# Performance work log

Measured on AMD Instinct MI355X. Metric: run time of the kernel, lower is better.

The kernel has to match this reference:

```python
import jax, jax.numpy as jnp
import numpy as np

N = 50000        # nodes
E = 1_000_000    # edges
F_IN = 128       # input features
H1, D1 = 8, 16   # layer-1 heads / per-head dim
D2 = 2           # layer-2 out dim (heads=1, concat=False)
NEG_SLOPE = 0.2  # PyG GATConv default leaky-relu slope


def setup_inputs() -> dict:
    key = jax.random.key(0)
    ks = jax.random.split(key, 10)
    x = jax.random.normal(ks[0], (N, F_IN), dtype=jnp.float32)
    edge_index = jax.random.randint(ks[1], (2, E), 0, N, dtype=jnp.int32)
    # layer 1 params: W1 maps F_IN -> H1*D1; attention vectors per head
    W1 = jax.random.normal(ks[2], (F_IN, H1 * D1), jnp.float32) * 0.1
    a_src1 = jax.random.normal(ks[3], (H1, D1), jnp.float32) * 0.1
    a_dst1 = jax.random.normal(ks[4], (H1, D1), jnp.float32) * 0.1
    b1 = jnp.zeros((H1 * D1,), jnp.float32)
    # layer 2 params: 128 -> 2, single head
    W2 = jax.random.normal(ks[5], (H1 * D1, 1 * D2), jnp.float32) * 0.1
    a_src2 = jax.random.normal(ks[6], (1, D2), jnp.float32) * 0.1
    a_dst2 = jax.random.normal(ks[7], (1, D2), jnp.float32) * 0.1
    b2 = jnp.zeros((D2,), jnp.float32)
    return {"x": x, "edge_index": edge_index,
            "W1": W1, "a_src1": a_src1, "a_dst1": a_dst1, "b1": b1,
            "W2": W2, "a_src2": a_src2, "a_dst2": a_dst2, "b2": b2}


def gat_layer(x, src, dst, W, a_s, a_d, b, concat):
    # PyG GATConv: h = xW (per head); e_ij = leaky_relu(a_s.h_j + a_d.h_i);
    # alpha = softmax over incoming edges of node i; out_i = sum alpha_ij h_j
    n = x.shape[0]
    heads, d = a_s.shape
    h = (x @ W).reshape(n, heads, d)                      # [N,H,D]
    es = jnp.einsum('nhd,hd->nh', h, a_s)                 # [N,H]
    ed = jnp.einsum('nhd,hd->nh', h, a_d)
    e = jax.nn.leaky_relu(es[src] + ed[dst], NEG_SLOPE)   # [E,H]
    m = jax.ops.segment_max(e, dst, num_segments=n)       # stable softmax max
    m = jnp.where(jnp.isfinite(m), m, 0.0)
    w = jnp.exp(e - m[dst])
    denom = jax.ops.segment_sum(w, dst, num_segments=n)
    alpha = w / (denom[dst] + 1e-16)                      # [E,H]
    out = jax.ops.segment_sum(alpha[:, :, None] * h[src], dst, num_segments=n)
    out = out.reshape(n, heads * d) if concat else out.mean(axis=1)
    return out + b


def reference(x, edge_index, W1, a_src1, a_dst1, b1, W2, a_src2, a_dst2, b2):
    n = x.shape[0]
    loops = jnp.arange(n, dtype=edge_index.dtype)         # add_self_loops (PyG default)
    src = jnp.concatenate([edge_index[0], loops])
    dst = jnp.concatenate([edge_index[1], loops])
    x1 = jax.nn.elu(gat_layer(x, src, dst, W1, a_src1, a_dst1, b1, concat=True))
    x2 = jax.nn.elu(gat_layer(x1, src, dst, W2, a_src2, a_dst2, b2, concat=False))
    return x2.mean(axis=0)                                # [2]
```

## Files before the change

kernel.cpp:

```cpp
#include <hip/hip_runtime.h>
#include <hip/hip_fp8.h>
#include <math.h>

#define NEG_SLOPE 0.2f
#define FD 128
#define H1 8
#define BSH 7
#define BWD 128
#define CAPE 3072
#define CAPC 3200
#define SCAP 3200
#define CHK 2048
#define XPAD 136
#define CURS 16
#define LOG2E 1.44269504088896f

#if defined(__has_builtin)
#if __has_builtin(__builtin_amdgcn_cvt_pk_f32_fp8) && __has_builtin(__builtin_amdgcn_cvt_pk_fp8_f32)
#define HW_FP8 1
#endif
#if __has_builtin(__builtin_amdgcn_exp2f)
#define HW_EXP2 1
#endif
#endif

typedef float v2f __attribute__((ext_vector_type(2)));
typedef short bf16x8 __attribute__((ext_vector_type(8)));
typedef float f32x4v __attribute__((ext_vector_type(4)));

__device__ inline float fexp2(float x) {
#ifdef HW_EXP2
    return __builtin_amdgcn_exp2f(x);
#else
    return exp2f(x);
#endif
}

__device__ inline unsigned char fp8_1(float v) {
#ifdef HW_FP8
    return (unsigned char)(__builtin_amdgcn_cvt_pk_fp8_f32(v, v, 0, false) & 0xff);
#else
    __hip_fp8_e4m3 q(v); return (unsigned char)q.__x;
#endif
}

template <bool HI>
__device__ inline v2f unpack2_fp8(unsigned int pk) {
#ifdef HW_FP8
    return __builtin_amdgcn_cvt_pk_f32_fp8((int)pk, HI);
#else
    __hip_fp8_e4m3 q0, q1;
    const int sh = HI ? 16 : 0;
    q0.__x = (__hip_fp8_storage_t)((pk >> sh) & 0xff);
    q1.__x = (__hip_fp8_storage_t)((pk >> (sh + 8)) & 0xff);
    v2f r; r.x = (float)q0; r.y = (float)q1;
    return r;
#endif
}

__device__ inline unsigned int pkbf2(float a, float b) {
    union { float f; unsigned u; } ua, ub;
    ua.f = a; ub.f = b;
    unsigned ra = (ua.u + 0x7FFF + ((ua.u >> 16) & 1)) >> 16;
    unsigned rb = (ub.u + 0x7FFF + ((ub.u >> 16) & 1)) >> 16;
    return (ra & 0xFFFFu) | (rb << 16);
}

__device__ inline unsigned short bf16_1(float a) {
    union { float f; unsigned u; } ua; ua.f = a;
    return (unsigned short)((ua.u + 0x7FFF + ((ua.u >> 16) & 1)) >> 16);
}


__global__ __launch_bounds__(256) void prep_kernel(
        const float* __restrict__ W1, const float* __restrict__ a_s,
        const float* __restrict__ a_d,
        unsigned short* __restrict__ W1t, unsigned short* __restrict__ wsd,
        int* __restrict__ cur, int nbk) {
    int t = blockIdx.x * 256 + threadIdx.x;
    if (t < FD * FD) {
        int k = t >> 7, n = t & 127;
        union { float f; unsigned u; } uu;
        uu.f = W1[t];
        unsigned r = (uu.u + 0x7FFF + ((uu.u >> 16) & 1)) >> 16;
        W1t[n * FD + k] = (unsigned short)r;
    }
    if (t < 16 * FD) {
        int j = t >> 7, k = t & 127;
        int head = j & 7;
        const float* av = (j < 8) ? (a_s + head * 16) : (a_d + head * 16);
        const float* wr = W1 + k * FD + head * 16;
        float v = 0.f;
        #pragma unroll
        for (int d = 0; d < 16; d++) v += wr[d] * av[d];
        v *= LOG2E;
        unsigned short hi = bf16_1(v);
        union { float f; unsigned u; } hf; hf.u = ((unsigned)hi) << 16;
        unsigned short lo = bf16_1(v - hf.f);
        wsd[j * FD + k] = hi;
        wsd[(16 + j) * FD + k] = lo;
    }
    if (t < nbk) cur[t * CURS] = t * CAPE;
}

union FusedSmem {
    struct {
        unsigned short xs[64 * XPAD];
    } g;
    int bucket[1024];
};

__global__ __launch_bounds__(256) void fused_gemm_bucketize_kernel(
        const float* __restrict__ x, const unsigned short* __restrict__ W1t,
        const unsigned short* __restrict__ wsd,
        unsigned char* __restrict__ h1, float* __restrict__ es1, float* __restrict__ ed1,
        int N, const int* __restrict__ ei, int E, int nbk,
        int* __restrict__ bkt_cursor, int* __restrict__ bkt_edges, int nchk) {
    __shared__ FusedSmem sm;
    const int tid = threadIdx.x;

    if ((int)blockIdx.x < nchk) {
        int* lcnt = sm.bucket;
        int* lbase = sm.bucket + nbk;
        for (int i = tid; i < nbk; i += 256) lcnt[i] = 0;
        __syncthreads();
        const int base = blockIdx.x * CHK;
        const int end = min(base + CHK, E);
        int info[CHK / 256];
        #pragma unroll
        for (int t = 0; t < CHK / 256; t++) {
            int i = base + tid + t * 256;
            info[t] = -1;
            if (i < end) {
                int b = ei[E + i] >> BSH;
                int r = atomicAdd(&lcnt[b], 1);
                info[t] = (r << 9) | b;
            }
        }
        __syncthreads();
        const int rot = (int)((blockIdx.x * 53u) % (unsigned)nbk);
        for (int i = tid; i < nbk; i += 256) {
            int b = i + rot; if (b >= nbk) b -= nbk;
            int c = lcnt[b];
            lbase[b] = c ? atomicAdd(&bkt_cursor[b * CURS], c) : 0;
        }
        __syncthreads();
        #pragma unroll
        for (int t = 0; t < CHK / 256; t++) {
            int i = base + tid + t * 256;
            if (info[t] >= 0) {
                int b = info[t] & 511;
                int r = info[t] >> 9;
                int pos = lbase[b] + r;
                if (pos < (b + 1) * CAPE) {
                    unsigned int src = (unsigned int)ei[i];
                    unsigned int dl = (unsigned int)(ei[E + i] & (BWD - 1));
                    bkt_edges[pos] = (int)(src | (dl << 25));
                }
            }
        }
        return;
    }

    const int tile = blockIdx.x - nchk;
    const int row0 = tile * 64;
    unsigned short* xs = sm.g.xs;

    #pragma unroll
    for (int it = 0; it < 8; ++it) {
        int idx = it * 256 + tid;
        int r   = idx >> 5;
        int c4  = idx & 31;
        int gr  = min(row0 + r, N - 1);
        float4 v = ((const float4*)(x + (size_t)gr * FD))[c4];
        unsigned int p0 = pkbf2(v.x, v.y);
        unsigned int p1 = pkbf2(v.z, v.w);
        *(unsigned int*)(xs + r * XPAD + c4 * 4) = p0;
        *(unsigned int*)(xs + r * XPAD + c4 * 4 + 2) = p1;
    }
    __syncthreads();

    const int wave = tid >> 6, lane = tid & 63;
    const int quad = lane >> 4, l16 = lane & 15;
    const int n0w = wave * 32;

    f32x4v acc[4][2];
    f32x4v acce;
    #pragma unroll
    for (int mt = 0; mt < 4; mt++)
        #pragma unroll
        for (int nt = 0; nt < 2; nt++)
            #pragma unroll
            for (int c = 0; c < 4; c++) acc[mt][nt][c] = 0.f;
    #pragma unroll
    for (int c = 0; c < 4; c++) acce[c] = 0.f;

    #pragma unroll
    for (int kt = 0; kt < 4; kt++) {
        const int kb = kt * 32 + quad * 8;
        bf16x8 a0 = *(const bf16x8*)(xs + (0 * 16 + l16) * XPAD + kb);
        bf16x8 a1 = *(const bf16x8*)(xs + (1 * 16 + l16) * XPAD + kb);
        bf16x8 a2 = *(const bf16x8*)(xs + (2 * 16 + l16) * XPAD + kb);
        bf16x8 a3 = *(const bf16x8*)(xs + (3 * 16 + l16) * XPAD + kb);
        bf16x8 b0 = *(const bf16x8*)(W1t + (n0w + 0 * 16 + l16) * FD + kb);
        bf16x8 b1 = *(const bf16x8*)(W1t + (n0w + 1 * 16 + l16) * FD + kb);
        bf16x8 bh = *(const bf16x8*)(wsd + (0 * 16 + l16) * FD + kb);
        bf16x8 bl = *(const bf16x8*)(wsd + (1 * 16 + l16) * FD + kb);
        acc[0][0] = __builtin_amdgcn_mfma_f32_16x16x32_bf16(a0, b0, acc[0][0], 0, 0, 0);
        acc[1][0] = __builtin_amdgcn_mfma_f32_16x16x32_bf16(a1, b0, acc[1][0], 0, 0, 0);
        acc[2][0] = __builtin_amdgcn_mfma_f32_16x16x32_bf16(a2, b0, acc[2][0], 0, 0, 0);
        acc[3][0] = __builtin_amdgcn_mfma_f32_16x16x32_bf16(a3, b0, acc[3][0], 0, 0, 0);
        acc[0][1] = __builtin_amdgcn_mfma_f32_16x16x32_bf16(a0, b1, acc[0][1], 0, 0, 0);
        acc[1][1] = __builtin_amdgcn_mfma_f32_16x16x32_bf16(a1, b1, acc[1][1], 0, 0, 0);
        acc[2][1] = __builtin_amdgcn_mfma_f32_16x16x32_bf16(a2, b1, acc[2][1], 0, 0, 0);
        acc[3][1] = __builtin_amdgcn_mfma_f32_16x16x32_bf16(a3, b1, acc[3][1], 0, 0, 0);
        if (wave == 0) {
            acce = __builtin_amdgcn_mfma_f32_16x16x32_bf16(a0, bh, acce, 0, 0, 0);
            acce = __builtin_amdgcn_mfma_f32_16x16x32_bf16(a0, bl, acce, 0, 0, 0);
        } else if (wave == 1) {
            acce = __builtin_amdgcn_mfma_f32_16x16x32_bf16(a1, bh, acce, 0, 0, 0);
            acce = __builtin_amdgcn_mfma_f32_16x16x32_bf16(a1, bl, acce, 0, 0, 0);
        } else if (wave == 2) {
            acce = __builtin_amdgcn_mfma_f32_16x16x32_bf16(a2, bh, acce, 0, 0, 0);
            acce = __builtin_amdgcn_mfma_f32_16x16x32_bf16(a2, bl, acce, 0, 0, 0);
        } else {
            acce = __builtin_amdgcn_mfma_f32_16x16x32_bf16(a3, bh, acce, 0, 0, 0);
            acce = __builtin_amdgcn_mfma_f32_16x16x32_bf16(a3, bl, acce, 0, 0, 0);
        }
    }

    #pragma unroll
    for (int reg = 0; reg < 4; reg++) {
        int row = row0 + wave * 16 + quad * 4 + reg;
        if (row < N) {
            float v = acce[reg];
            if (l16 < 8) es1[row * H1 + l16] = v;
            else         ed1[row * H1 + (l16 - 8)] = v;
        }
    }

    #pragma unroll
    for (int nt = 0; nt < 2; nt++) {
        const int col = n0w + nt * 16 + l16;
        #pragma unroll
        for (int mt = 0; mt < 4; mt++) {
            #pragma unroll
            for (int reg = 0; reg < 4; reg++) {
                int row = row0 + mt * 16 + quad * 4 + reg;
                if (row < N) h1[(size_t)row * FD + col] = fp8_1(acc[mt][nt][reg]);
            }
        }
    }
}

__global__ __launch_bounds__(256) void sort2_kernel(
        const int* __restrict__ bkt_cursor, const int* __restrict__ bkt_edges,
        int* __restrict__ csr_src, int* __restrict__ rowstart,
        int* __restrict__ rowend, int N) {
    __shared__ int lcnt[BWD];
    __shared__ int lcur[BWD];
    __shared__ int stage[SCAP];
    __shared__ int sorted[SCAP];
    const int b = blockIdx.x;
    const int n0 = b << BSH;
    const int nb = min(BWD, N - n0);
    const int s = b * CAPE;
    const int cnt = min(bkt_cursor[b * CURS] - s, CAPE);
    const int region = b * CAPC;
    const int tid = threadIdx.x;

    if (tid < BWD) lcnt[tid] = (tid < nb) ? 1 : 0;
    __syncthreads();
    for (int i = tid; i < cnt; i += 256) {
        int v = bkt_edges[s + i];
        stage[i] = v;
        atomicAdd(&lcnt[((unsigned int)v) >> 25], 1);
    }
    __syncthreads();
    if (tid < 64) {
        int carry = 0;
        #pragma unroll
        for (int half = 0; half < 2; half++) {
            int i = half * 64 + tid;
            int v = lcnt[i];
            int incl = v;
            #pragma unroll
            for (int off = 1; off < 64; off <<= 1) {
                int t = __shfl_up(incl, off);
                if (tid >= off) incl += t;
            }
            lcur[i] = carry + incl - v;
            carry += __shfl(incl, 63);
        }
    }
    __syncthreads();
    if (tid < nb) {
        int p = lcur[tid];
        rowstart[n0 + tid] = region + p;
        rowend[n0 + tid] = region + p + lcnt[tid];
        sorted[p] = n0 + tid;
        lcur[tid] = p + 1;
    }
    __syncthreads();
    for (int i = tid; i < cnt; i += 256) {
        int v = stage[i];
        int dl = ((unsigned int)v) >> 25;
        int src = v & 0x1FFFFFF;
        int pos = atomicAdd(&lcur[dl], 1);
        sorted[pos] = src;
    }
    __syncthreads();
    const int total = cnt + nb;
    for (int i = total + tid; i < CAPC; i += 256) sorted[i] = 0;
    __syncthreads();
    int4* dst4 = (int4*)(csr_src + region);
    const int4* src4 = (const int4*)sorted;
    for (int i = tid; i < CAPC / 4; i += 256) dst4[i] = src4[i];
}

__global__ __launch_bounds__(256) void agg1_kernel(
        const unsigned int* __restrict__ h1, const float* __restrict__ es1,
        const float* __restrict__ ed1,
        const int* __restrict__ rowstart, const int* __restrict__ rowend,
        const int* __restrict__ csr_src,
        const float* __restrict__ b1, const float* __restrict__ W2,
        const float* __restrict__ a_s2, const float* __restrict__ a_d2,
        float* __restrict__ h2, float* __restrict__ es2, float* __restrict__ ed2, int N) {
    const int j = threadIdx.x;
    const int q = j & 31;
    const int h = q >> 2;
    const int n = blockIdx.x * 8 + (j >> 5);
    const bool valid = (n < N);

    int s = 0, e = 0;
    float edh = 0.f;
    if (valid) {
        s = rowstart[n];
        e = rowend[n];
        edh = ed1[(n << 3) + h];
    }
    int nbat = (e - s + 31) >> 5;
    int nmax = max(nbat, __shfl_xor(nbat, 32));

    float acc0 = 0.f, acc1 = 0.f, acc2 = 0.f, acc3 = 0.f, wsum = 0.f;
    for (int k = 0; k < nmax; ++k) {
        int base = s + (k << 5);
        int cm = min(e - base, 32);
        int myidx = csr_src[base + q];
        myidx = min(max(myidx, 0), N - 1);
        int cl = max(cm - 1, 0);
        int cmax = max(cm, __shfl_xor(cm, 32));
        for (int t = 0; t < cmax; t += 8) {
            int i0 = min(t, cl),     i1 = min(t + 1, cl);
            int i2 = min(t + 2, cl), i3 = min(t + 3, cl);
            int i4 = min(t + 4, cl), i5 = min(t + 5, cl);
            int i6 = min(t + 6, cl), i7 = min(t + 7, cl);
            int s0 = __shfl(myidx, i0, 32);
            int s1 = __shfl(myidx, i1, 32);
            int s2 = __shfl(myidx, i2, 32);
            int s3 = __shfl(myidx, i3, 32);
            int s4 = __shfl(myidx, i4, 32);
            int s5 = __shfl(myidx, i5, 32);
            int s6 = __shfl(myidx, i6, 32);
            int s7 = __shfl(myidx, i7, 32);
            float g0 = es1[(s0 << 3) + h];
            float g1 = es1[(s1 << 3) + h];
            float g2 = es1[(s2 << 3) + h];
            float g3 = es1[(s3 << 3) + h];
            float g4 = es1[(s4 << 3) + h];
            float g5 = es1[(s5 << 3) + h];
            float g6 = es1[(s6 << 3) + h];
            float g7 = es1[(s7 << 3) + h];
            unsigned int p0 = h1[(s0 << 5) + q];
            unsigned int p1 = h1[(s1 << 5) + q];
            unsigned int p2 = h1[(s2 << 5) + q];
            unsigned int p3 = h1[(s3 << 5) + q];
            unsigned int p4 = h1[(s4 << 5) + q];
            unsigned int p5 = h1[(s5 << 5) + q];
            unsigned int p6 = h1[(s6 << 5) + q];
            unsigned int p7 = h1[(s7 << 5) + q];
            g0 += edh; g1 += edh; g2 += edh; g3 += edh;
            g4 += edh; g5 += edh; g6 += edh; g7 += edh;
            g0 = fmaxf(g0, g0 * NEG_SLOPE);
            g1 = fmaxf(g1, g1 * NEG_SLOPE);
            g2 = fmaxf(g2, g2 * NEG_SLOPE);
            g3 = fmaxf(g3, g3 * NEG_SLOPE);
            g4 = fmaxf(g4, g4 * NEG_SLOPE);
            g5 = fmaxf(g5, g5 * NEG_SLOPE);
            g6 = fmaxf(g6, g6 * NEG_SLOPE);
            g7 = fmaxf(g7, g7 * NEG_SLOPE);
            float w0 = (t     < cm) ? fexp2(g0) : 0.f;
            float w1 = (t + 1 < cm) ? fexp2(g1) : 0.f;
            float w2 = (t + 2 < cm) ? fexp2(g2) : 0.f;
            float w3 = (t + 3 < cm) ? fexp2(g3) : 0.f;
            float w4 = (t + 4 < cm) ? fexp2(g4) : 0.f;
            float w5 = (t + 5 < cm) ? fexp2(g5) : 0.f;
            float w6 = (t + 6 < cm) ? fexp2(g6) : 0.f;
            float w7 = (t + 7 < cm) ? fexp2(g7) : 0.f;
            v2f a01 = unpack2_fp8<false>(p0), a23 = unpack2_fp8<true>(p0);
            v2f b01 = unpack2_fp8<false>(p1), b23 = unpack2_fp8<true>(p1);
            v2f c01 = unpack2_fp8<false>(p2), c23 = unpack2_fp8<true>(p2);
            v2f d01 = unpack2_fp8<false>(p3), d23 = unpack2_fp8<true>(p3);
            v2f e01 = unpack2_fp8<false>(p4), e23 = unpack2_fp8<true>(p4);
            v2f f01 = unpack2_fp8<false>(p5), f23 = unpack2_fp8<true>(p5);
            v2f g01 = unpack2_fp8<false>(p6), g23 = unpack2_fp8<true>(p6);
            v2f h01 = unpack2_fp8<false>(p7), h23 = unpack2_fp8<true>(p7);
            acc0 += w0 * a01.x; acc1 += w0 * a01.y; acc2 += w0 * a23.x; acc3 += w0 * a23.y;
            acc0 += w1 * b01.x; acc1 += w1 * b01.y; acc2 += w1 * b23.x; acc3 += w1 * b23.y;
            acc0 += w2 * c01.x; acc1 += w2 * c01.y; acc2 += w2 * c23.x; acc3 += w2 * c23.y;
            acc0 += w3 * d01.x; acc1 += w3 * d01.y; acc2 += w3 * d23.x; acc3 += w3 * d23.y;
            acc0 += w4 * e01.x; acc1 += w4 * e01.y; acc2 += w4 * e23.x; acc3 += w4 * e23.y;
            acc0 += w5 * f01.x; acc1 += w5 * f01.y; acc2 += w5 * f23.x; acc3 += w5 * f23.y;
            acc0 += w6 * g01.x; acc1 += w6 * g01.y; acc2 += w6 * g23.x; acc3 += w6 * g23.y;
            acc0 += w7 * h01.x; acc1 += w7 * h01.y; acc2 += w7 * h23.x; acc3 += w7 * h23.y;
            wsum += (w0 + w1) + (w2 + w3) + (w4 + w5) + (w6 + w7);
        }
    }

    float inv = 1.f / wsum;
    float4 bv = *(const float4*)&b1[4 * q];
    float x0 = acc0 * inv + bv.x;
    float x1 = acc1 * inv + bv.y;
    float x2 = acc2 * inv + bv.z;
    float x3 = acc3 * inv + bv.w;
    x0 = (x0 > 0.f) ? x0 : expm1f(x0);
    x1 = (x1 > 0.f) ? x1 : expm1f(x1);
    x2 = (x2 > 0.f) ? x2 : expm1f(x2);
    x3 = (x3 > 0.f) ? x3 : expm1f(x3);

    float4 w2a = *(const float4*)&W2[8 * q];
    float4 w2b = *(const float4*)&W2[8 * q + 4];
    float c0 = x0 * w2a.x + x1 * w2a.z + x2 * w2b.x + x3 * w2b.z;
    float c1 = x0 * w2a.y + x1 * w2a.w + x2 * w2b.y + x3 * w2b.w;
    #pragma unroll
    for (int m = 1; m < 32; m <<= 1) {
        c0 += __shfl_xor(c0, m);
        c1 += __shfl_xor(c1, m);
    }
    if (q == 0 && valid) {
        h2[(size_t)n * 2 + 0] = c0;
        h2[(size_t)n * 2 + 1] = c1;
        es2[n] = LOG2E * (c0 * a_s2[0] + c1 * a_s2[1]);
        ed2[n] = LOG2E * (c0 * a_d2[0] + c1 * a_d2[1]);
    }
}

__global__ __launch_bounds__(256) void agg2_kernel(
        const float* __restrict__ h2, const float* __restrict__ es2, const float* __restrict__ ed2,
        const int* __restrict__ rowstart, const int* __restrict__ rowend,
        const int* __restrict__ csr_src,
        const float* __restrict__ b2, float* __restrict__ partial, int N) {
    const int g = threadIdx.x >> 5, lane = threadIdx.x & 31;
    const int n = blockIdx.x * 8 + g;
    float v0 = 0.f, v1 = 0.f;
    if (n < N) {
        const float ed = ed2[n];
        const int s = rowstart[n], e = rowend[n];
        float a0 = 0.f, a1 = 0.f, ws = 0.f;
        for (int i = s + lane; i < e; i += 32) {
            int src = csr_src[i];
            float t = es2[src] + ed;
            float w = fexp2(fmaxf(t, t * NEG_SLOPE));
            a0 += w * h2[(size_t)src * 2 + 0];
            a1 += w * h2[(size_t)src * 2 + 1];
            ws += w;
        }
        #pragma unroll
        for (int m = 1; m < 32; m <<= 1) {
            a0 += __shfl_xor(a0, m, 32);
            a1 += __shfl_xor(a1, m, 32);
            ws += __shfl_xor(ws, m, 32);
        }
        if (lane == 0) {
            v0 = a0 / ws + b2[0]; v0 = (v0 > 0.f) ? v0 : expm1f(v0);
            v1 = a1 / ws + b2[1]; v1 = (v1 > 0.f) ? v1 : expm1f(v1);
        }
    }
    __shared__ float buf[16];
    if (lane == 0) { buf[g * 2] = v0; buf[g * 2 + 1] = v1; }
    __syncthreads();
    if (threadIdx.x == 0) {
        float s0 = 0.f, s1 = 0.f;
        #pragma unroll
        for (int i = 0; i < 8; i++) { s0 += buf[2 * i]; s1 += buf[2 * i + 1]; }
        partial[(size_t)blockIdx.x * 2 + 0] = s0;
        partial[(size_t)blockIdx.x * 2 + 1] = s1;
    }
}

__global__ __launch_bounds__(256) void final_reduce_kernel(
        const float* __restrict__ partial, int nb, float invN, float* __restrict__ out) {
    const int tid = threadIdx.x, lane = tid & 63, wv = tid >> 6;
    float s0 = 0.f, s1 = 0.f;
    for (int i = tid; i < nb; i += 256) { s0 += partial[2 * i]; s1 += partial[2 * i + 1]; }
    #pragma unroll
    for (int m = 1; m < 64; m <<= 1) { s0 += __shfl_xor(s0, m); s1 += __shfl_xor(s1, m); }
    __shared__ float buf[8];
    if (lane == 0) { buf[wv * 2] = s0; buf[wv * 2 + 1] = s1; }
    __syncthreads();
    if (tid == 0) {
        out[0] = (buf[0] + buf[2] + buf[4] + buf[6]) * invN;
        out[1] = (buf[1] + buf[3] + buf[5] + buf[7]) * invN;
    }
}

extern "C" void kernel_launch(void* const* d_in, const int* in_sizes, int n_in,
                              void* d_out, int out_size, void* d_ws, size_t ws_size,
                              hipStream_t stream) {
    const float* x    = (const float*)d_in[0];
    const int*   ei   = (const int*)  d_in[1];
    const float* W1   = (const float*)d_in[2];
    const float* a_s1 = (const float*)d_in[3];
    const float* a_d1 = (const float*)d_in[4];
    const float* b1   = (const float*)d_in[5];
    const float* W2   = (const float*)d_in[6];
    const float* a_s2 = (const float*)d_in[7];
    const float* a_d2 = (const float*)d_in[8];
    const float* b2   = (const float*)d_in[9];
    float* out = (float*)d_out;

    const int N = in_sizes[0] / FD;
    const int E = in_sizes[1] / 2;
    const int nbk  = (N + BWD - 1) >> BSH;
    const int nchk = (E + CHK - 1) / CHK;
    const int ngemm = (N + 63) / 64;

    char* wp = (char*)d_ws;
    auto carve = [&](size_t bytes) {
        char* p = wp;
        wp += (bytes + 255) & ~(size_t)255;
        return p;
    };
    unsigned char* h1 = (unsigned char*)carve((size_t)N * FD);
    float* es1      = (float*)carve((size_t)N * H1 * 4);
    float* ed1      = (float*)carve((size_t)N * H1 * 4);
    int*   rowstart = (int*)  carve((size_t)N * 4);
    int*   rowend   = (int*)  carve((size_t)N * 4);
    int*   csr_src  = (int*)  carve(((size_t)nbk * CAPC + CAPC) * 4);
    int*   bkt_cursor = (int*)carve((size_t)nbk * CURS * 4);
    int*   bkt_edges  = (int*)carve((size_t)nbk * CAPE * 4);
    unsigned short* W1t = (unsigned short*)carve((size_t)FD * FD * 2);
    unsigned short* wsd = (unsigned short*)carve((size_t)32 * FD * 2);
    float* h2       = (float*)carve((size_t)N * 2 * 4);
    float* es2      = (float*)carve((size_t)N * 4);
    float* ed2      = (float*)carve((size_t)N * 4);
    const int nb2   = (N + 7) / 8;
    float* partial  = (float*)carve((size_t)nb2 * 2 * 4);

    prep_kernel<<<(FD * FD + 255) / 256, 256, 0, stream>>>(W1, a_s1, a_d1, W1t, wsd,
                                                           bkt_cursor, nbk);

    fused_gemm_bucketize_kernel<<<nchk + ngemm, 256, 0, stream>>>(
        x, W1t, wsd, h1, es1, ed1, N, ei, E, nbk, bkt_cursor, bkt_edges, nchk);

    sort2_kernel<<<nbk, 256, 0, stream>>>(bkt_cursor, bkt_edges, csr_src, rowstart, rowend, N);

    agg1_kernel<<<(N + 7) / 8, 256, 0, stream>>>((const unsigned int*)h1, es1, ed1,
                                                 rowstart, rowend, csr_src,
                                                 b1, W2, a_s2, a_d2, h2, es2, ed2, N);

    agg2_kernel<<<(N + 7) / 8, 256, 0, stream>>>(h2, es2, ed2, rowstart, rowend, csr_src,
                                                 b2, partial, N);
    final_reduce_kernel<<<1, 256, 0, stream>>>(partial, nb2, 1.0f / (float)N, out);
}
```

Before: 184.4 us.

## Split layer-1 aggregation into two head-half passes over split feature buffers

The fp8 h1 features and es1 scores are stored as two separate half-width arrays (heads 0-3 and heads 4-7). Layer-1 aggregation then runs as two kernel launches, one per half, each using 16 lanes per node, with the partial layer-2 projection carried through a workspace buffer between passes. The goal is to shrink each pass's random-gather working set (3.2 MB of h1 per half) so it fits better in cache. The cost is reading the CSR indices and row ranges twice, an extra launch, and an extra round trip for the partial sums. Index loads are also changed to nontemporal loads.

Result: slower. 194.8 us (+5.6%).

```diff
diff --git a/kernel.cpp b/kernel.cpp
--- a/kernel.cpp
+++ b/kernel.cpp
@@ -113,7 +113,8 @@
 __global__ __launch_bounds__(256) void fused_gemm_bucketize_kernel(
         const float* __restrict__ x, const unsigned short* __restrict__ W1t,
         const unsigned short* __restrict__ wsd,
-        unsigned char* __restrict__ h1, float* __restrict__ es1, float* __restrict__ ed1,
+        unsigned char* __restrict__ h1a, unsigned char* __restrict__ h1b,
+        float* __restrict__ es1a, float* __restrict__ es1b, float* __restrict__ ed1,
         int N, const int* __restrict__ ei, int E, int nbk,
         int* __restrict__ bkt_cursor, int* __restrict__ bkt_edges, int nchk) {
     __shared__ FusedSmem sm;
@@ -234,20 +235,22 @@
         int row = row0 + wave * 16 + quad * 4 + reg;
         if (row < N) {
             float v = acce[reg];
-            if (l16 < 8) es1[row * H1 + l16] = v;
-            else         ed1[row * H1 + (l16 - 8)] = v;
-        }
-    }
-
+            if (l16 < 4)       es1a[row * 4 + l16] = v;
+            else if (l16 < 8)  es1b[row * 4 + (l16 - 4)] = v;
+            else               ed1[row * H1 + (l16 - 8)] = v;
+        }
+    }
+
+    unsigned char* __restrict__ hdst = (wave < 2) ? h1a : h1b;
     #pragma unroll
     for (int nt = 0; nt < 2; nt++) {
-        const int col = n0w + nt * 16 + l16;
+        const int col = (n0w + nt * 16 + l16) & 63;
         #pragma unroll
         for (int mt = 0; mt < 4; mt++) {
             #pragma unroll
             for (int reg = 0; reg < 4; reg++) {
                 int row = row0 + mt * 16 + quad * 4 + reg;
-                if (row < N) h1[(size_t)row * FD + col] = fp8_1(acc[mt][nt][reg]);
+                if (row < N) hdst[(size_t)row * 64 + col] = fp8_1(acc[mt][nt][reg]);
             }
         }
     }
@@ -318,18 +321,21 @@
     for (int i = tid; i < CAPC / 4; i += 256) dst4[i] = src4[i];
 }
 
-__global__ __launch_bounds__(256) void agg1_kernel(
-        const unsigned int* __restrict__ h1, const float* __restrict__ es1,
+template <int PASS>
+__global__ __launch_bounds__(256) void agg1_pass_kernel(
+        const unsigned int* __restrict__ h1h,
+        const float* __restrict__ esh,
         const float* __restrict__ ed1,
         const int* __restrict__ rowstart, const int* __restrict__ rowend,
         const int* __restrict__ csr_src,
         const float* __restrict__ b1, const float* __restrict__ W2,
         const float* __restrict__ a_s2, const float* __restrict__ a_d2,
-        float* __restrict__ h2, float* __restrict__ es2, float* __restrict__ ed2, int N) {
-    const int j = threadIdx.x;
-    const int q = j & 31;
-    const int h = q >> 2;
-    const int n = blockIdx.x * 8 + (j >> 5);
+        float* __restrict__ pc,
+        float* __restrict__ h2, float* __restrict__ es2, float* __restrict__ ed2,
+        int N) {
+    const int q4 = threadIdx.x & 15;
+    const int h  = q4 >> 2;
+    const int n  = blockIdx.x * 16 + (threadIdx.x >> 4);
     const bool valid = (n < N);
 
     int s = 0, e = 0;
@@ -337,48 +343,46 @@
     if (valid) {
         s = rowstart[n];
         e = rowend[n];
-        edh = ed1[(n << 3) + h];
-    }
-    int nbat = (e - s + 31) >> 5;
-    int nmax = max(nbat, __shfl_xor(nbat, 32));
+        edh = ed1[(n << 3) + PASS * 4 + h];
+    }
+    const int nbat = (e - s + 15) >> 4;
 
     float acc0 = 0.f, acc1 = 0.f, acc2 = 0.f, acc3 = 0.f, wsum = 0.f;
-    for (int k = 0; k < nmax; ++k) {
-        int base = s + (k << 5);
-        int cm = min(e - base, 32);
-        int myidx = csr_src[base + q];
+    for (int k = 0; k < nbat; ++k) {
+        int base = s + (k << 4);
+        int cm = min(e - base, 16);
+        int myidx = __builtin_nontemporal_load(csr_src + base + q4);
         myidx = min(max(myidx, 0), N - 1);
         int cl = max(cm - 1, 0);
-        int cmax = max(cm, __shfl_xor(cm, 32));
-        for (int t = 0; t < cmax; t += 8) {
+        for (int t = 0; t < cm; t += 8) {
             int i0 = min(t, cl),     i1 = min(t + 1, cl);
             int i2 = min(t + 2, cl), i3 = min(t + 3, cl);
             int i4 = min(t + 4, cl), i5 = min(t + 5, cl);
             int i6 = min(t + 6, cl), i7 = min(t + 7, cl);
-            int s0 = __shfl(myidx, i0, 32);
-            int s1 = __shfl(myidx, i1, 32);
-            int s2 = __shfl(myidx, i2, 32);
-            int s3 = __shfl(myidx, i3, 32);
-            int s4 = __shfl(myidx, i4, 32);
-            int s5 = __shfl(myidx, i5, 32);
-            int s6 = __shfl(myidx, i6, 32);
-            int s7 = __shfl(myidx, i7, 32);
-            float g0 = es1[(s0 << 3) + h];
-            float g1 = es1[(s1 << 3) + h];
-            float g2 = es1[(s2 << 3) + h];
-            float g3 = es1[(s3 << 3) + h];
-            float g4 = es1[(s4 << 3) + h];
-            float g5 = es1[(s5 << 3) + h];
-            float g6 = es1[(s6 << 3) + h];
-            float g7 = es1[(s7 << 3) + h];
-            unsigned int p0 = h1[(s0 << 5) + q];
-            unsigned int p1 = h1[(s1 << 5) + q];
-            unsigned int p2 = h1[(s2 << 5) + q];
-            unsigned int p3 = h1[(s3 << 5) + q];
-            unsigned int p4 = h1[(s4 << 5) + q];
-            unsigned int p5 = h1[(s5 << 5) + q];
-            unsigned int p6 = h1[(s6 << 5) + q];
-            unsigned int p7 = h1[(s7 << 5) + q];
+            int s0 = __shfl(myidx, i0, 16);
+            int s1 = __shfl(myidx, i1, 16);
+            int s2 = __shfl(myidx, i2, 16);
+            int s3 = __shfl(myidx, i3, 16);
+            int s4 = __shfl(myidx, i4, 16);
+            int s5 = __shfl(myidx, i5, 16);
+            int s6 = __shfl(myidx, i6, 16);
+            int s7 = __shfl(myidx, i7, 16);
+            float g0 = esh[(s0 << 2) + h];
+            float g1 = esh[(s1 << 2) + h];
+            float g2 = esh[(s2 << 2) + h];
+            float g3 = esh[(s3 << 2) + h];
+            float g4 = esh[(s4 << 2) + h];
+            float g5 = esh[(s5 << 2) + h];
+            float g6 = esh[(s6 << 2) + h];
+            float g7 = esh[(s7 << 2) + h];
+            unsigned int p0 = h1h[(s0 << 4) + q4];
+            unsigned int p1 = h1h[(s1 << 4) + q4];
+            unsigned int p2 = h1h[(s2 << 4) + q4];
+            unsigned int p3 = h1h[(s3 << 4) + q4];
+            unsigned int p4 = h1h[(s4 << 4) + q4];
+            unsigned int p5 = h1h[(s5 << 4) + q4];
+            unsigned int p6 = h1h[(s6 << 4) + q4];
+            unsigned int p7 = h1h[(s7 << 4) + q4];
             g0 += edh; g1 += edh; g2 += edh; g3 += edh;
             g4 += edh; g5 += edh; g6 += edh; g7 += edh;
             g0 = fmaxf(g0, g0 * NEG_SLOPE);
@@ -417,8 +421,9 @@
         }
     }
 
+    const int FB = PASS * 64;
     float inv = 1.f / wsum;
-    float4 bv = *(const float4*)&b1[4 * q];
+    float4 bv = *(const float4*)&b1[FB + 4 * q4];
     float x0 = acc0 * inv + bv.x;
     float x1 = acc1 * inv + bv.y;
     float x2 = acc2 * inv + bv.z;
@@ -428,20 +433,27 @@
     x2 = (x2 > 0.f) ? x2 : expm1f(x2);
     x3 = (x3 > 0.f) ? x3 : expm1f(x3);
 
-    float4 w2a = *(const float4*)&W2[8 * q];
-    float4 w2b = *(const float4*)&W2[8 * q + 4];
+    float4 w2a = *(const float4*)&W2[2 * FB + 8 * q4];
+    float4 w2b = *(const float4*)&W2[2 * FB + 8 * q4 + 4];
     float c0 = x0 * w2a.x + x1 * w2a.z + x2 * w2b.x + x3 * w2b.z;
     float c1 = x0 * w2a.y + x1 * w2a.w + x2 * w2b.y + x3 * w2b.w;
     #pragma unroll
-    for (int m = 1; m < 32; m <<= 1) {
-        c0 += __shfl_xor(c0, m);
-        c1 += __shfl_xor(c1, m);
-    }
-    if (q == 0 && valid) {
-        h2[(size_t)n * 2 + 0] = c0;
-        h2[(size_t)n * 2 + 1] = c1;
-        es2[n] = LOG2E * (c0 * a_s2[0] + c1 * a_s2[1]);
-        ed2[n] = LOG2E * (c0 * a_d2[0] + c1 * a_d2[1]);
+    for (int m = 1; m < 16; m <<= 1) {
+        c0 += __shfl_xor(c0, m, 16);
+        c1 += __shfl_xor(c1, m, 16);
+    }
+    if (q4 == 0 && valid) {
+        if (PASS == 0) {
+            pc[(size_t)n * 2 + 0] = c0;
+            pc[(size_t)n * 2 + 1] = c1;
+        } else {
+            c0 += pc[(size_t)n * 2 + 0];
+            c1 += pc[(size_t)n * 2 + 1];
+            h2[(size_t)n * 2 + 0] = c0;
+            h2[(size_t)n * 2 + 1] = c1;
+            es2[n] = LOG2E * (c0 * a_s2[0] + c1 * a_s2[1]);
+            ed2[n] = LOG2E * (c0 * a_d2[0] + c1 * a_d2[1]);
+        }
     }
 }
 
@@ -531,8 +543,10 @@
         wp += (bytes + 255) & ~(size_t)255;
         return p;
     };
-    unsigned char* h1 = (unsigned char*)carve((size_t)N * FD);
-    float* es1      = (float*)carve((size_t)N * H1 * 4);
+    unsigned char* h1a = (unsigned char*)carve((size_t)N * 64);
+    unsigned char* h1b = (unsigned char*)carve((size_t)N * 64);
+    float* es1a     = (float*)carve((size_t)N * 4 * 4);
+    float* es1b     = (float*)carve((size_t)N * 4 * 4);
     float* ed1      = (float*)carve((size_t)N * H1 * 4);
     int*   rowstart = (int*)  carve((size_t)N * 4);
     int*   rowend   = (int*)  carve((size_t)N * 4);
@@ -541,6 +555,7 @@
     int*   bkt_edges  = (int*)carve((size_t)nbk * CAPE * 4);
     unsigned short* W1t = (unsigned short*)carve((size_t)FD * FD * 2);
     unsigned short* wsd = (unsigned short*)carve((size_t)32 * FD * 2);
+    float* pc       = (float*)carve((size_t)N * 2 * 4);
     float* h2       = (float*)carve((size_t)N * 2 * 4);
     float* es2      = (float*)carve((size_t)N * 4);
     float* ed2      = (float*)carve((size_t)N * 4);
@@ -551,13 +566,20 @@
                                                            bkt_cursor, nbk);
 
     fused_gemm_bucketize_kernel<<<nchk + ngemm, 256, 0, stream>>>(
-        x, W1t, wsd, h1, es1, ed1, N, ei, E, nbk, bkt_cursor, bkt_edges, nchk);
+        x, W1t, wsd, h1a, h1b, es1a, es1b, ed1, N, ei, E, nbk,
+        bkt_cursor, bkt_edges, nchk);
 
     sort2_kernel<<<nbk, 256, 0, stream>>>(bkt_cursor, bkt_edges, csr_src, rowstart, rowend, N);
 
-    agg1_kernel<<<(N + 7) / 8, 256, 0, stream>>>((const unsigned int*)h1, es1, ed1,
-                                                 rowstart, rowend, csr_src,
-                                                 b1, W2, a_s2, a_d2, h2, es2, ed2, N);
+    const int nagg = (N + 15) / 16;
+    agg1_pass_kernel<0><<<nagg, 256, 0, stream>>>((const unsigned int*)h1a, es1a, ed1,
+                                                  rowstart, rowend, csr_src,
+                                                  b1, W2, a_s2, a_d2,
+                                                  pc, h2, es2, ed2, N);
+    agg1_pass_kernel<1><<<nagg, 256, 0, stream>>>((const unsigned int*)h1b, es1b, ed1,
+                                                  rowstart, rowend, csr_src,
+                                                  b1, W2, a_s2, a_d2,
+                                                  pc, h2, es2, ed2, N);
 
     agg2_kernel<<<(N + 7) / 8, 256, 0, stream>>>(h2, es2, ed2, rowstart, rowend, csr_src,
                                                  b2, partial, N);
```
